# Optimization experiments

Hardware: AMD Instinct MI355X
Metric: run time of the kernel (lower is better)

## Reference

```python
import jax, jax.numpy as jnp
import numpy as np

N_NODES = 100000
N_INCID = 2000000
HIDDEN = 128
N_HE = 100000


def setup_inputs() -> dict:
    key = jax.random.key(0)
    k1, k2, k3 = jax.random.split(key, 3)
    node_feats = jax.random.normal(k1, (N_NODES, HIDDEN), dtype=jnp.float32)
    hyperedge_index = jax.random.randint(k2, (2, N_INCID), 0, N_HE, dtype=jnp.int64)
    # xavier_uniform for Linear(hidden,1): bound = sqrt(6/(hidden+1))
    bound = float(np.sqrt(6.0 / (HIDDEN + 1)))
    W = jax.random.uniform(k3, (1, HIDDEN), dtype=jnp.float32, minval=-bound, maxval=bound)
    return {"node_feats": node_feats, "hyperedge_index": hyperedge_index,
            "num_hyperedges": N_HE, "W": W}


def reference(node_feats, hyperedge_index, num_hyperedges, W):
    node_idx = hyperedge_index[0]
    he_idx = hyperedge_index[1]
    gathered = node_feats[node_idx]                      # [E, D]
    scores = jnp.einsum('ed,d->e', gathered, W[0])       # [E]
    # segment softmax over hyperedges
    seg_max = jax.ops.segment_max(scores, he_idx, num_segments=num_hyperedges)
    seg_max = jnp.where(jnp.isfinite(seg_max), seg_max, 0.0)  # empty segments
    w = jnp.exp(scores - seg_max[he_idx])                # [E]
    denom = jax.ops.segment_sum(w, he_idx, num_segments=num_hyperedges)
    w_norm = w / jnp.maximum(denom, 1e-20)[he_idx]       # [E]
    # weighted scatter-sum; empty hyperedges stay zero
    out = jax.ops.segment_sum(w_norm[:, None] * gathered, he_idx,
                              num_segments=num_hyperedges)  # [H, D]
    return out
```

## Files before the change

kernel.cpp:

```cpp
#include <hip/hip_runtime.h>
#include <hip/hip_fp16.h>
#include <math.h>

#define N_NODES 100000
#define N_INCID 2000000
#define HIDDEN  128
#define N_HE    100000

#define CHAINS 4
#define EPB 1024
#define FILL_BLOCKS ((N_INCID + EPB - 1) / EPB)
#define PREP_BLOCKS ((N_NODES + 3) / 4)

typedef float vf4 __attribute__((ext_vector_type(4)));

__device__ inline float4 h4_to_f4(uint2 p) {
    __half2 a = *(__half2*)&p.x;
    __half2 b = *(__half2*)&p.y;
    float2 fa = __half22float2(a);
    float2 fb = __half22float2(b);
    return make_float4(fa.x, fa.y, fb.x, fb.y);
}

__global__ void prep_fill_kernel(const float* __restrict__ nf,
                                 const float* __restrict__ W,
                                 const int* __restrict__ idx,
                                 float* __restrict__ en,
                                 __half2* __restrict__ nfh2,
                                 int* __restrict__ head,
                                 int2* __restrict__ next8) {
    int b = blockIdx.x;
    if (b < FILL_BLOCKS) {
        int base = b * EPB;
        int e = base + threadIdx.x;
        if (base + EPB <= N_INCID) {
            int he[4], nd[4], prev[4];
            #pragma unroll
            for (int k = 0; k < 4; ++k) {
                he[k] = idx[N_INCID + e + 256 * k];
                nd[k] = idx[e + 256 * k];
            }
            #pragma unroll
            for (int k = 0; k < 4; ++k) {
                int ek = e + 256 * k;
                prev[k] = atomicExch(&head[(he[k] << 2) | (ek & 3)], ek);
            }
            #pragma unroll
            for (int k = 0; k < 4; ++k)
                next8[e + 256 * k] = make_int2(nd[k], prev[k]);
        } else {
            #pragma unroll
            for (int k = 0; k < 4; ++k) {
                int ek = e + 256 * k;
                if (ek < N_INCID) {
                    int he = idx[N_INCID + ek];
                    int nd = idx[ek];
                    int prev = atomicExch(&head[(he << 2) | (ek & 3)], ek);
                    next8[ek] = make_int2(nd, prev);
                }
            }
        }
    } else {
        int wave = threadIdx.x >> 6, lane = threadIdx.x & 63;
        int n = (b - FILL_BLOCKS) * 4 + wave;
        if (n >= N_NODES) return;
        const float2* nf2 = (const float2*)nf;
        const float2* w2  = (const float2*)W;
        float2 v = nf2[(size_t)n * 64 + lane];
        float2 w = w2[lane];
        float p = v.x * w.x + v.y * w.y;
        #pragma unroll
        for (int o = 32; o > 0; o >>= 1) p += __shfl_xor(p, o, 64);
        if (lane == 0) en[n] = __expf(p);
        nfh2[(size_t)n * 64 + lane] = __floats2half2_rn(v.x, v.y);
    }
}

__global__ void compute_kernel_h(const int* __restrict__ head,
                                 const int2* __restrict__ next8,
                                 const float* __restrict__ en,
                                 const uint2* __restrict__ nfh4,
                                 float* __restrict__ out) {
    int wave = threadIdx.x >> 6, lane = threadIdx.x & 63;
    int half = lane >> 5, l32 = lane & 31;
    int he = blockIdx.x * 8 + wave * 2 + half;
    if (he >= N_HE) return;

    const long long* __restrict__ nxt = (const long long*)next8;

    int4 h4 = ((const int4*)head)[he];
    int e0 = h4.x, e1 = h4.y, e2 = h4.z, e3 = h4.w;

    float4 acc = make_float4(0.f, 0.f, 0.f, 0.f);
    float denom = 0.f;

    while ((e0 & e1 & e2 & e3) != -1) {
        long long q0 = nxt[e0 < 0 ? 0 : e0];
        long long q1 = nxt[e1 < 0 ? 0 : e1];
        long long q2 = nxt[e2 < 0 ? 0 : e2];
        long long q3 = nxt[e3 < 0 ? 0 : e3];

        int n0 = (int)q0, n1 = (int)q1, n2 = (int)q2, n3 = (int)q3;

        float w0 = en[n0]; w0 = (e0 >= 0) ? w0 : 0.f;
        float w1 = en[n1]; w1 = (e1 >= 0) ? w1 : 0.f;
        float w2 = en[n2]; w2 = (e2 >= 0) ? w2 : 0.f;
        float w3 = en[n3]; w3 = (e3 >= 0) ? w3 : 0.f;

        float4 v0 = h4_to_f4(nfh4[(size_t)n0 * 32 + l32]);
        float4 v1 = h4_to_f4(nfh4[(size_t)n1 * 32 + l32]);
        float4 v2 = h4_to_f4(nfh4[(size_t)n2 * 32 + l32]);
        float4 v3 = h4_to_f4(nfh4[(size_t)n3 * 32 + l32]);

        acc.x += w0 * v0.x + w1 * v1.x + w2 * v2.x + w3 * v3.x;
        acc.y += w0 * v0.y + w1 * v1.y + w2 * v2.y + w3 * v3.y;
        acc.z += w0 * v0.z + w1 * v1.z + w2 * v2.z + w3 * v3.z;
        acc.w += w0 * v0.w + w1 * v1.w + w2 * v2.w + w3 * v3.w;
        denom += (w0 + w1) + (w2 + w3);

        e0 = (e0 >= 0) ? (int)(q0 >> 32) : -1;
        e1 = (e1 >= 0) ? (int)(q1 >> 32) : -1;
        e2 = (e2 >= 0) ? (int)(q2 >> 32) : -1;
        e3 = (e3 >= 0) ? (int)(q3 >> 32) : -1;
    }

    float inv = 1.0f / fmaxf(denom, 1e-20f);
    acc.x *= inv; acc.y *= inv; acc.z *= inv; acc.w *= inv;
    vf4 accv = { acc.x, acc.y, acc.z, acc.w };
    __builtin_nontemporal_store(accv, (vf4*)&((float4*)out)[(size_t)he * 32 + l32]);
}

extern "C" void kernel_launch(void* const* d_in, const int* in_sizes, int n_in,
                              void* d_out, int out_size, void* d_ws, size_t ws_size,
                              hipStream_t stream) {
    const float* nf  = (const float*)d_in[0];
    const int*   idx = (const int*)d_in[1];
    const float* W   = (const float*)d_in[3];
    float* out = (float*)d_out;
    char* ws = (char*)d_ws;

    int*     head  = (int*)(ws + 0);
    float*   en    = (float*)(ws + 1600000);
    __half2* nfh2  = (__half2*)(ws + 2000000);
    int2*    next8 = (int2*)(ws + 27600000);

    hipMemsetAsync(head, 0xFF, CHAINS * N_HE * sizeof(int), stream);
    prep_fill_kernel<<<FILL_BLOCKS + PREP_BLOCKS, 256, 0, stream>>>(
        nf, W, idx, en, nfh2, head, next8);
    compute_kernel_h<<<(N_HE + 7) / 8, 256, 0, stream>>>(
        head, next8, en, (const uint2*)nfh2, out);
}
```

Before: 320.1 us.

## Assign one wave per hyperedge with one 16-lane group per chain

```diff
diff --git a/kernel.cpp b/kernel.cpp
--- a/kernel.cpp
+++ b/kernel.cpp
@@ -14,9 +14,9 @@
 
 typedef float vf4 __attribute__((ext_vector_type(4)));
 
-__device__ inline float4 h4_to_f4(uint2 p) {
-    __half2 a = *(__half2*)&p.x;
-    __half2 b = *(__half2*)&p.y;
+__device__ inline float4 h4_to_f4(unsigned a_, unsigned b_) {
+    __half2 a = *(__half2*)&a_;
+    __half2 b = *(__half2*)&b_;
     float2 fa = __half22float2(a);
     float2 fb = __half22float2(b);
     return make_float4(fa.x, fa.y, fb.x, fb.y);
@@ -76,58 +76,54 @@
     }
 }
 
-__global__ void compute_kernel_h(const int* __restrict__ head,
+__global__ void compute_kernel_w(const int* __restrict__ head,
                                  const int2* __restrict__ next8,
                                  const float* __restrict__ en,
-                                 const uint2* __restrict__ nfh4,
+                                 const uint4* __restrict__ nfq,
                                  float* __restrict__ out) {
     int wave = threadIdx.x >> 6, lane = threadIdx.x & 63;
-    int half = lane >> 5, l32 = lane & 31;
-    int he = blockIdx.x * 8 + wave * 2 + half;
-    if (he >= N_HE) return;
+    int he = blockIdx.x * 4 + wave;
+    int q16 = lane >> 4, l16 = lane & 15;
 
     const long long* __restrict__ nxt = (const long long*)next8;
 
-    int4 h4 = ((const int4*)head)[he];
-    int e0 = h4.x, e1 = h4.y, e2 = h4.z, e3 = h4.w;
+    int e = head[(he << 2) | q16];
+    float4 acc0 = make_float4(0.f, 0.f, 0.f, 0.f);
+    float4 acc1 = make_float4(0.f, 0.f, 0.f, 0.f);
+    float den = 0.f;
 
-    float4 acc = make_float4(0.f, 0.f, 0.f, 0.f);
-    float denom = 0.f;
-
-    while ((e0 & e1 & e2 & e3) != -1) {
-        long long q0 = nxt[e0 < 0 ? 0 : e0];
-        long long q1 = nxt[e1 < 0 ? 0 : e1];
-        long long q2 = nxt[e2 < 0 ? 0 : e2];
-        long long q3 = nxt[e3 < 0 ? 0 : e3];
-
-        int n0 = (int)q0, n1 = (int)q1, n2 = (int)q2, n3 = (int)q3;
-
-        float w0 = en[n0]; w0 = (e0 >= 0) ? w0 : 0.f;
-        float w1 = en[n1]; w1 = (e1 >= 0) ? w1 : 0.f;
-        float w2 = en[n2]; w2 = (e2 >= 0) ? w2 : 0.f;
-        float w3 = en[n3]; w3 = (e3 >= 0) ? w3 : 0.f;
-
-        float4 v0 = h4_to_f4(nfh4[(size_t)n0 * 32 + l32]);
-        float4 v1 = h4_to_f4(nfh4[(size_t)n1 * 32 + l32]);
-        float4 v2 = h4_to_f4(nfh4[(size_t)n2 * 32 + l32]);
-        float4 v3 = h4_to_f4(nfh4[(size_t)n3 * 32 + l32]);
-
-        acc.x += w0 * v0.x + w1 * v1.x + w2 * v2.x + w3 * v3.x;
-        acc.y += w0 * v0.y + w1 * v1.y + w2 * v2.y + w3 * v3.y;
-        acc.z += w0 * v0.z + w1 * v1.z + w2 * v2.z + w3 * v3.z;
-        acc.w += w0 * v0.w + w1 * v1.w + w2 * v2.w + w3 * v3.w;
-        denom += (w0 + w1) + (w2 + w3);
-
-        e0 = (e0 >= 0) ? (int)(q0 >> 32) : -1;
-        e1 = (e1 >= 0) ? (int)(q1 >> 32) : -1;
-        e2 = (e2 >= 0) ? (int)(q2 >> 32) : -1;
-        e3 = (e3 >= 0) ? (int)(q3 >> 32) : -1;
+    while (e >= 0) {
+        long long q = nxt[e];
+        int nd = (int)q;
+        float w = en[nd];
+        uint4 r = nfq[(size_t)nd * 16 + l16];
+        float4 a = h4_to_f4(r.x, r.y);
+        float4 bq = h4_to_f4(r.z, r.w);
+        acc0.x += w * a.x;  acc0.y += w * a.y;
+        acc0.z += w * a.z;  acc0.w += w * a.w;
+        acc1.x += w * bq.x; acc1.y += w * bq.y;
+        acc1.z += w * bq.z; acc1.w += w * bq.w;
+        den += w;
+        e = (int)(q >> 32);
     }
 
-    float inv = 1.0f / fmaxf(denom, 1e-20f);
-    acc.x *= inv; acc.y *= inv; acc.z *= inv; acc.w *= inv;
-    vf4 accv = { acc.x, acc.y, acc.z, acc.w };
-    __builtin_nontemporal_store(accv, (vf4*)&((float4*)out)[(size_t)he * 32 + l32]);
+    #pragma unroll
+    for (int o = 16; o <= 32; o <<= 1) {
+        acc0.x += __shfl_xor(acc0.x, o, 64); acc0.y += __shfl_xor(acc0.y, o, 64);
+        acc0.z += __shfl_xor(acc0.z, o, 64); acc0.w += __shfl_xor(acc0.w, o, 64);
+        acc1.x += __shfl_xor(acc1.x, o, 64); acc1.y += __shfl_xor(acc1.y, o, 64);
+        acc1.z += __shfl_xor(acc1.z, o, 64); acc1.w += __shfl_xor(acc1.w, o, 64);
+        den += __shfl_xor(den, o, 64);
+    }
+
+    if (lane < 16) {
+        float inv = 1.0f / fmaxf(den, 1e-20f);
+        vf4 o0 = { acc0.x * inv, acc0.y * inv, acc0.z * inv, acc0.w * inv };
+        vf4 o1 = { acc1.x * inv, acc1.y * inv, acc1.z * inv, acc1.w * inv };
+        float* op = out + (size_t)he * 128 + l16 * 8;
+        __builtin_nontemporal_store(o0, (vf4*)op);
+        __builtin_nontemporal_store(o1, (vf4*)(op + 4));
+    }
 }
 
 extern "C" void kernel_launch(void* const* d_in, const int* in_sizes, int n_in,
@@ -147,6 +143,6 @@
     hipMemsetAsync(head, 0xFF, CHAINS * N_HE * sizeof(int), stream);
     prep_fill_kernel<<<FILL_BLOCKS + PREP_BLOCKS, 256, 0, stream>>>(
         nf, W, idx, en, nfh2, head, next8);
-    compute_kernel_h<<<(N_HE + 7) / 8, 256, 0, stream>>>(
-        head, next8, en, (const uint2*)nfh2, out);
+    compute_kernel_w<<<(N_HE + 3) / 4, 256, 0, stream>>>(
+        head, next8, en, (const uint4*)nfh2, out);
 }
```

Measured after the change: 310.7 us. -2.9%, faster.
